# Kernel tuning notes

Measured on AMD Instinct MI355X. Metric: run time of the kernel, lower is better.

Reference implementation:

```python
import jax, jax.numpy as jnp
import numpy as np

B, T, X, E, H, L = 4096, 32, 256, 32, 512, 2  # batch, theta_size, x_size, n_masks, hidden, num_hidden_layers


def _prelu(v, a):
    # PReLU with per-channel slope a (broadcast [E,H] or [B,E,H] vs [B,E,H])
    return jnp.where(v >= 0, v, a * v)


def setup_inputs() -> dict:
    key = jax.random.key(0)
    ks = jax.random.split(key, 12)
    theta = jax.random.normal(ks[0], (B, T), dtype=jnp.float32)
    x = jax.random.normal(ks[1], (B, X), dtype=jnp.float32)
    masks = jax.random.randint(ks[2], (E, T), 0, 2, dtype=jnp.int32)
    masks = masks.at[:, 0].set(1)  # guarantee non-empty subsets
    D = T + X
    s_in = 1.0 / np.sqrt(D)
    s_h = 1.0 / np.sqrt(H)
    # first Linear, split into theta-part and x-part of the weight matrix
    W1t = jax.random.normal(ks[3], (E, T, H), dtype=jnp.float32) * s_in
    W1x = jax.random.normal(ks[4], (E, X, H), dtype=jnp.float32) * s_in
    b1 = jax.random.normal(ks[5], (E, H), dtype=jnp.float32) * s_in
    a1 = jnp.full((E, H), 0.25, dtype=jnp.float32)  # PReLU init
    # num_layers hidden Linear(H,H) + PReLU
    Wh = jax.random.normal(ks[6], (L, E, H, H), dtype=jnp.float32) * s_h
    bh = jax.random.normal(ks[7], (L, E, H), dtype=jnp.float32) * s_h
    ah = jnp.full((L, E, H), 0.25, dtype=jnp.float32)
    # output Linear(H, 1) -> squeeze(-1)
    Wo = jax.random.normal(ks[8], (E, H), dtype=jnp.float32) * s_h
    bo = jax.random.normal(ks[9], (E,), dtype=jnp.float32) * s_h
    return {"theta": theta, "x": x, "masks": masks, "W1t": W1t, "W1x": W1x,
            "b1": b1, "a1": a1, "Wh": Wh, "bh": bh, "ah": ah, "Wo": Wo, "bo": bo}


def reference(theta, x, masks, W1t, W1x, b1, a1, Wh, bh, ah, Wo, bo):
    # theta[..., mask] followed by Linear is equivalent to masking theta per
    # expert and contracting with the full per-expert theta weight block.
    m = masks.astype(theta.dtype)                      # [E, T]
    tm = theta[:, None, :] * m[None, :, :]             # [B, E, T]
    h = (jnp.einsum('bet,eth->beh', tm, W1t)
         + jnp.einsum('bx,exh->beh', x, W1x) + b1)     # [B, E, H]
    h = _prelu(h, a1)
    for i in range(Wh.shape[0]):                       # small fixed layer loop
        h = jnp.einsum('beh,ehk->bek', h, Wh[i]) + bh[i]
        h = _prelu(h, ah[i])
    # Linear(H,1).squeeze(-1), stacked over masks on the last dim -> [B, E]
    return jnp.einsum('beh,eh->be', h, Wo) + bo
```

## Files before the change

### kernel.cpp

```cpp
#include <hip/hip_runtime.h>
#include <stdint.h>

#define B_SZ 4096
#define T_SZ 32
#define X_SZ 256
#define E_SZ 32
#define H_SZ 512
#define BM   64
#define AROW 1040

typedef __attribute__((ext_vector_type(8))) short  short8;
typedef __attribute__((ext_vector_type(4))) float  floatx4;

__device__ __forceinline__ unsigned pk2(float a, float b) {
  unsigned r;
  asm("v_cvt_pk_bf16_f32 %0, %1, %2" : "=v"(r) : "v"(a), "v"(b));
  return r;
}

__global__ __launch_bounds__(256) void prep_kernel(
    const float* __restrict__ W1t, const float* __restrict__ W1x,
    const int* __restrict__ masks, const float* __restrict__ Wh,
    uint4* __restrict__ wcat, uint4* __restrict__ whf) {
  __shared__ unsigned lds[16 * 516];
  const int c = blockIdx.x;
  const int t = threadIdx.x;

  const float* base;
  bool needMask = false;
  int e1 = 0;
  if (c >= 288) {
    int cc = c - 288;
    int le = cc >> 4, kt = cc & 15;
    base = Wh + ((size_t)le * H_SZ + kt * 32) * H_SZ;
  } else {
    int e = c / 9, kt = c - e * 9;
    e1 = e;
    if (kt == 0) { base = W1t + (size_t)e * T_SZ * H_SZ; needMask = true; }
    else          base = W1x + ((size_t)e * X_SZ + (kt - 1) * 32) * H_SZ;
  }

#pragma unroll
  for (int i = 0; i < 8; ++i) {
    int g  = i * 256 + t;
    int k2 = g >> 7, np = g & 127;
    const float* r0 = base + (size_t)(2 * k2) * H_SZ + np * 4;
    float4 a = *(const float4*)r0;
    float4 b = *(const float4*)(r0 + H_SZ);
    if (needMask) {
      float s0 = (float)masks[e1 * T_SZ + 2 * k2];
      float s1 = (float)masks[e1 * T_SZ + 2 * k2 + 1];
      a.x *= s0; a.y *= s0; a.z *= s0; a.w *= s0;
      b.x *= s1; b.y *= s1; b.z *= s1; b.w *= s1;
    }
    *(uint4*)&lds[k2 * 516 + np * 4] =
        make_uint4(pk2(a.x, b.x), pk2(a.y, b.y), pk2(a.z, b.z), pk2(a.w, b.w));
  }
  __syncthreads();

  uint4* outp = (c < 288) ? (wcat + (size_t)c * 2048)
                          : (whf + (size_t)(c - 288) * 2048);
  const int w = t >> 6, l = t & 63, q = l >> 4, l16 = l & 15;
#pragma unroll
  for (int j = 0; j < 8; ++j) {
    int nb = w * 8 + j;
    int n  = nb * 16 + l16;
    int kb = 4 * q;
    uint4 v;
    v.x = lds[(kb + 0) * 516 + n];
    v.y = lds[(kb + 1) * 516 + n];
    v.z = lds[(kb + 2) * 516 + n];
    v.w = lds[(kb + 3) * 516 + n];
    outp[nb * 64 + l] = v;
  }
}

__global__ __launch_bounds__(512, 4) void mlp_kernel(
    const float* __restrict__ theta, const float* __restrict__ x,
    const short8* __restrict__ wcat, const short8* __restrict__ whf,
    const float* __restrict__ b1, const float* __restrict__ a1,
    const float* __restrict__ bh, const float* __restrict__ ah,
    const float* __restrict__ Wo, const float* __restrict__ bo,
    float* __restrict__ out) {
  __shared__ __align__(16) char smA[BM * AROW];
  const int tid = threadIdx.x;
  const int bid = blockIdx.x;
  const int xcd = bid & 7;
  const int t8  = bid >> 3;
  const int e   = xcd * 4 + (t8 >> 6);
  const int m0  = (t8 & 63) * BM;
  const int w   = tid >> 6, l = tid & 63, l16 = l & 15, quad = l >> 4;

  {
    int r = tid >> 3, c = tid & 7;
    float4 th = *(const float4*)(theta + (size_t)(m0 + r) * T_SZ + c * 4);
    *(uint2*)(smA + r * AROW + c * 8) = make_uint2(pk2(th.x, th.y), pk2(th.z, th.w));
    const float4* xp = (const float4*)(x + (size_t)(m0 + r) * X_SZ + c * 32);
#pragma unroll
    for (int q = 0; q < 4; ++q) {
      float4 a = xp[q * 2], b = xp[q * 2 + 1];
      *(uint4*)(smA + r * AROW + 64 + c * 64 + q * 16) =
          make_uint4(pk2(a.x, a.y), pk2(a.z, a.w), pk2(b.x, b.y), pk2(b.z, b.w));
    }
  }
  __syncthreads();

  floatx4 acc[4][4];

  auto gemm = [&](const short8* wbase, int nkt) {
#pragma unroll
    for (int mb = 0; mb < 4; ++mb)
#pragma unroll
      for (int i = 0; i < 4; ++i) acc[mb][i] = (floatx4)(0.f);
    short8 bcur[4], bnxt[4];
    const int boff = w * 256 + l;
#pragma unroll
    for (int i = 0; i < 4; ++i) bcur[i] = wbase[boff + i * 64];
    for (int kt = 0; kt < nkt; ++kt) {
      const short8* wn = wbase + (size_t)(kt + 1 < nkt ? kt + 1 : kt) * 2048;
#pragma unroll
      for (int i = 0; i < 4; ++i) bnxt[i] = wn[boff + i * 64];
      short8 af[4];
#pragma unroll
      for (int mb = 0; mb < 4; ++mb)
        af[mb] = *(const short8*)(smA + (mb * 16 + l16) * AROW + kt * 64 + quad * 16);
#pragma unroll
      for (int mb = 0; mb < 4; ++mb)
#pragma unroll
        for (int i = 0; i < 4; ++i)
          acc[mb][i] = __builtin_amdgcn_mfma_f32_16x16x32_bf16(af[mb], bcur[i],
                                                               acc[mb][i], 0, 0, 0);
#pragma unroll
      for (int i = 0; i < 4; ++i) bcur[i] = bnxt[i];
    }
  };

  auto epi_store = [&](const float* bias, const float* slope) {
    float bb[4], aa[4];
#pragma unroll
    for (int i = 0; i < 4; ++i) {
      int col = w * 64 + i * 16 + l16;
      bb[i] = bias[col];
      aa[i] = slope[col];
    }
    __syncthreads();
#pragma unroll
    for (int mb = 0; mb < 4; ++mb) {
#pragma unroll
      for (int i = 0; i < 4; ++i) {
        unsigned dw[4];
#pragma unroll
        for (int r = 0; r < 4; ++r) {
          float v = acc[mb][i][r] + bb[i];
          v = v >= 0.f ? v : aa[i] * v;
          float o  = __shfl_xor(v, 1, 64);
          float lo = (l16 & 1) ? o : v;
          float hi = (l16 & 1) ? v : o;
          dw[r] = pk2(lo, hi);
        }
        int col2  = w * 64 + i * 16 + (l16 & ~1);
        int rbase = (l16 & 1) * 2;
#pragma unroll
        for (int rr = 0; rr < 2; ++rr) {
          int row = mb * 16 + quad * 4 + rbase + rr;
          *(unsigned*)(smA + row * AROW + col2 * 2) = dw[rbase + rr];
        }
      }
    }
    __syncthreads();
  };

  gemm(wcat + (size_t)e * 9 * 2048, 9);
  epi_store(b1 + (size_t)e * H_SZ, a1 + (size_t)e * H_SZ);
  gemm(whf + (size_t)e * 16 * 2048, 16);
  epi_store(bh + (size_t)e * H_SZ, ah + (size_t)e * H_SZ);
  gemm(whf + (size_t)(E_SZ + e) * 16 * 2048, 16);
  {
    float bb[4], aa[4], wo[4];
#pragma unroll
    for (int i = 0; i < 4; ++i) {
      int col = w * 64 + i * 16 + l16;
      bb[i] = bh[(size_t)(E_SZ + e) * H_SZ + col];
      aa[i] = ah[(size_t)(E_SZ + e) * H_SZ + col];
      wo[i] = Wo[(size_t)e * H_SZ + col];
    }
    float ps[4][4];
#pragma unroll
    for (int mb = 0; mb < 4; ++mb)
#pragma unroll
      for (int r = 0; r < 4; ++r) ps[mb][r] = 0.f;
#pragma unroll
    for (int mb = 0; mb < 4; ++mb)
#pragma unroll
      for (int i = 0; i < 4; ++i)
#pragma unroll
        for (int r = 0; r < 4; ++r) {
          float v = acc[mb][i][r] + bb[i];
          v = v >= 0.f ? v : aa[i] * v;
          ps[mb][r] += v * wo[i];
        }
#pragma unroll
    for (int d = 1; d < 16; d <<= 1)
#pragma unroll
      for (int mb = 0; mb < 4; ++mb)
#pragma unroll
        for (int r = 0; r < 4; ++r) ps[mb][r] += __shfl_xor(ps[mb][r], d, 64);
    __syncthreads();
    float* scratch = (float*)smA;
    if (l16 == 0) {
#pragma unroll
      for (int mb = 0; mb < 4; ++mb)
#pragma unroll
        for (int r = 0; r < 4; ++r)
          scratch[(mb * 16 + quad * 4 + r) * 8 + w] = ps[mb][r];
    }
    __syncthreads();
    if (tid < BM) {
      float s = 0.f;
#pragma unroll
      for (int ww = 0; ww < 8; ++ww) s += scratch[tid * 8 + ww];
      out[(size_t)(m0 + tid) * E_SZ + e] = s + bo[e];
    }
  }
}

extern "C" void kernel_launch(void* const* d_in, const int* in_sizes, int n_in,
                              void* d_out, int out_size, void* d_ws, size_t ws_size,
                              hipStream_t stream) {
  const float* theta = (const float*)d_in[0];
  const float* x     = (const float*)d_in[1];
  const int*   masks = (const int*)d_in[2];
  const float* W1t   = (const float*)d_in[3];
  const float* W1x   = (const float*)d_in[4];
  const float* b1    = (const float*)d_in[5];
  const float* a1    = (const float*)d_in[6];
  const float* Wh    = (const float*)d_in[7];
  const float* bh    = (const float*)d_in[8];
  const float* ah    = (const float*)d_in[9];
  const float* Wo    = (const float*)d_in[10];
  const float* bo    = (const float*)d_in[11];
  float* out = (float*)d_out;

  uint4* wcat = (uint4*)d_ws;
  uint4* whf  = (uint4*)((char*)d_ws + (size_t)E_SZ * 9 * 2048 * 16);

  prep_kernel<<<1312, 256, 0, stream>>>(W1t, W1x, masks, Wh, wcat, whf);
  mlp_kernel<<<2048, 512, 0, stream>>>(theta, x, (const short8*)wcat,
                                       (const short8*)whf, b1, a1, bh, ah, Wo, bo,
                                       out);
}
```

Measured before the change: 319.0 us.

## Stagger per-wave K-loop start and interleave expert block mapping

```diff
diff --git a/kernel.cpp b/kernel.cpp
--- a/kernel.cpp
+++ b/kernel.cpp
@@ -87,8 +87,10 @@
   const int bid = blockIdx.x;
   const int xcd = bid & 7;
   const int t8  = bid >> 3;
-  const int e   = xcd * 4 + (t8 >> 6);
-  const int m0  = (t8 & 63) * BM;
+  const int pr  = t8 >> 7;
+  const int qq  = t8 & 127;
+  const int e   = xcd * 4 + pr * 2 + (qq & 1);
+  const int m0  = (qq >> 1) * BM;
   const int w   = tid >> 6, l = tid & 63, l16 = l & 15, quad = l >> 4;
 
   {
@@ -107,23 +109,28 @@
 
   floatx4 acc[4][4];
 
-  auto gemm = [&](const short8* wbase, int nkt) {
+  auto gemm = [&](const short8* wbase, int nkt, int start) {
 #pragma unroll
     for (int mb = 0; mb < 4; ++mb)
 #pragma unroll
       for (int i = 0; i < 4; ++i) acc[mb][i] = (floatx4)(0.f);
+    const int boff = w * 256 + l;
+    const short8* wp = wbase + (size_t)start * 2048 + boff;
     short8 bcur[4], bnxt[4];
-    const int boff = w * 256 + l;
-#pragma unroll
-    for (int i = 0; i < 4; ++i) bcur[i] = wbase[boff + i * 64];
-    for (int kt = 0; kt < nkt; ++kt) {
-      const short8* wn = wbase + (size_t)(kt + 1 < nkt ? kt + 1 : kt) * 2048;
-#pragma unroll
-      for (int i = 0; i < 4; ++i) bnxt[i] = wn[boff + i * 64];
+#pragma unroll
+    for (int i = 0; i < 4; ++i) bcur[i] = wp[i * 64];
+    int kt = start;
+    const char* arow = smA + l16 * AROW + quad * 16;
+    for (int j = 0; j < nkt; ++j) {
+      int ktn = kt + 1;
+      const short8* wpn = wp + 2048;
+      if (ktn == nkt) { ktn = 0; wpn = wbase + boff; }
+#pragma unroll
+      for (int i = 0; i < 4; ++i) bnxt[i] = wpn[i * 64];
       short8 af[4];
 #pragma unroll
       for (int mb = 0; mb < 4; ++mb)
-        af[mb] = *(const short8*)(smA + (mb * 16 + l16) * AROW + kt * 64 + quad * 16);
+        af[mb] = *(const short8*)(arow + mb * (16 * AROW) + kt * 64);
 #pragma unroll
       for (int mb = 0; mb < 4; ++mb)
 #pragma unroll
@@ -132,6 +139,8 @@
                                                                acc[mb][i], 0, 0, 0);
 #pragma unroll
       for (int i = 0; i < 4; ++i) bcur[i] = bnxt[i];
+      wp = wpn;
+      kt = ktn;
     }
   };
 
@@ -170,11 +179,11 @@
     __syncthreads();
   };
 
-  gemm(wcat + (size_t)e * 9 * 2048, 9);
+  gemm(wcat + (size_t)e * 9 * 2048, 9, (w * 9) >> 3);
   epi_store(b1 + (size_t)e * H_SZ, a1 + (size_t)e * H_SZ);
-  gemm(whf + (size_t)e * 16 * 2048, 16);
+  gemm(whf + (size_t)e * 16 * 2048, 16, w * 2);
   epi_store(bh + (size_t)e * H_SZ, ah + (size_t)e * H_SZ);
-  gemm(whf + (size_t)(E_SZ + e) * 16 * 2048, 16);
+  gemm(whf + (size_t)(E_SZ + e) * 16 * 2048, 16, w * 2);
   {
     float bb[4], aa[4], wo[4];
 #pragma unroll
```

After: 321.5 us. About the same (+0.8%).

## Double row tile to 128 and fully unroll GEMM with ping-pong weight buffers

Applied to the files above, without the earlier changes.

```diff
diff --git a/kernel.cpp b/kernel.cpp
--- a/kernel.cpp
+++ b/kernel.cpp
@@ -1,12 +1,13 @@
 #include <hip/hip_runtime.h>
 #include <stdint.h>
+#include <type_traits>
 
 #define B_SZ 4096
 #define T_SZ 32
 #define X_SZ 256
 #define E_SZ 32
 #define H_SZ 512
-#define BM   64
+#define BM   128
 #define AROW 1040
 
 typedef __attribute__((ext_vector_type(8))) short  short8;
@@ -75,7 +76,7 @@
   }
 }
 
-__global__ __launch_bounds__(512, 4) void mlp_kernel(
+__global__ __launch_bounds__(512, 2) void mlp_kernel(
     const float* __restrict__ theta, const float* __restrict__ x,
     const short8* __restrict__ wcat, const short8* __restrict__ whf,
     const float* __restrict__ b1, const float* __restrict__ a1,
@@ -87,51 +88,69 @@
   const int bid = blockIdx.x;
   const int xcd = bid & 7;
   const int t8  = bid >> 3;
-  const int e   = xcd * 4 + (t8 >> 6);
-  const int m0  = (t8 & 63) * BM;
+  const int e   = xcd * 4 + (t8 >> 5);
+  const int m0  = (t8 & 31) * BM;
   const int w   = tid >> 6, l = tid & 63, l16 = l & 15, quad = l >> 4;
 
   {
-    int r = tid >> 3, c = tid & 7;
-    float4 th = *(const float4*)(theta + (size_t)(m0 + r) * T_SZ + c * 4);
-    *(uint2*)(smA + r * AROW + c * 8) = make_uint2(pk2(th.x, th.y), pk2(th.z, th.w));
-    const float4* xp = (const float4*)(x + (size_t)(m0 + r) * X_SZ + c * 32);
-#pragma unroll
-    for (int q = 0; q < 4; ++q) {
-      float4 a = xp[q * 2], b = xp[q * 2 + 1];
-      *(uint4*)(smA + r * AROW + 64 + c * 64 + q * 16) =
+    int r = tid >> 2, c = tid & 3;
+    const float* tp = theta + (size_t)(m0 + r) * T_SZ + c * 8;
+    float4 t0 = *(const float4*)tp;
+    float4 t1 = *(const float4*)(tp + 4);
+    *(uint4*)(smA + r * AROW + c * 16) =
+        make_uint4(pk2(t0.x, t0.y), pk2(t0.z, t0.w), pk2(t1.x, t1.y), pk2(t1.z, t1.w));
+    const float* xp = x + (size_t)(m0 + r) * X_SZ + c * 64;
+#pragma unroll
+    for (int j = 0; j < 8; ++j) {
+      float4 a = *(const float4*)(xp + j * 8);
+      float4 b = *(const float4*)(xp + j * 8 + 4);
+      *(uint4*)(smA + r * AROW + 64 + c * 128 + j * 16) =
           make_uint4(pk2(a.x, a.y), pk2(a.z, a.w), pk2(b.x, b.y), pk2(b.z, b.w));
     }
   }
   __syncthreads();
 
-  floatx4 acc[4][4];
-
-  auto gemm = [&](const short8* wbase, int nkt) {
-#pragma unroll
-    for (int mb = 0; mb < 4; ++mb)
+  floatx4 acc[8][4];
+  const int u0 = w * 256 + l;
+  const char* ar0 = smA + l16 * AROW + quad * 16;
+  const char* ar1 = ar0 + 4 * 16 * AROW;
+
+  auto gemm = [&](const short8* wbase, auto nktc) {
+    constexpr int NKT = decltype(nktc)::value;
+#pragma unroll
+    for (int mb = 0; mb < 8; ++mb)
 #pragma unroll
       for (int i = 0; i < 4; ++i) acc[mb][i] = (floatx4)(0.f);
-    short8 bcur[4], bnxt[4];
-    const int boff = w * 256 + l;
-#pragma unroll
-    for (int i = 0; i < 4; ++i) bcur[i] = wbase[boff + i * 64];
-    for (int kt = 0; kt < nkt; ++kt) {
-      const short8* wn = wbase + (size_t)(kt + 1 < nkt ? kt + 1 : kt) * 2048;
-#pragma unroll
-      for (int i = 0; i < 4; ++i) bnxt[i] = wn[boff + i * 64];
-      short8 af[4];
+    const short8* wu = wbase;
+    short8 bA[4], bB[4];
+#pragma unroll
+    for (int i = 0; i < 4; ++i) bA[i] = wu[u0 + i * 64];
+#pragma unroll
+    for (int kt = 0; kt < NKT; ++kt) {
+      if (kt + 1 < NKT) {
+        const short8* wn = wu + 2048;
+        if (kt & 1) {
+#pragma unroll
+          for (int i = 0; i < 4; ++i) bA[i] = wn[u0 + i * 64];
+        } else {
+#pragma unroll
+          for (int i = 0; i < 4; ++i) bB[i] = wn[u0 + i * 64];
+        }
+      }
+      short8 af[8];
 #pragma unroll
       for (int mb = 0; mb < 4; ++mb)
-        af[mb] = *(const short8*)(smA + (mb * 16 + l16) * AROW + kt * 64 + quad * 16);
+        af[mb] = *(const short8*)(ar0 + mb * (16 * AROW) + kt * 64);
 #pragma unroll
       for (int mb = 0; mb < 4; ++mb)
+        af[mb + 4] = *(const short8*)(ar1 + mb * (16 * AROW) + kt * 64);
+#pragma unroll
+      for (int mb = 0; mb < 8; ++mb)
 #pragma unroll
         for (int i = 0; i < 4; ++i)
-          acc[mb][i] = __builtin_amdgcn_mfma_f32_16x16x32_bf16(af[mb], bcur[i],
-                                                               acc[mb][i], 0, 0, 0);
-#pragma unroll
-      for (int i = 0; i < 4; ++i) bcur[i] = bnxt[i];
+          acc[mb][i] = __builtin_amdgcn_mfma_f32_16x16x32_bf16(
+              af[mb], (kt & 1) ? bB[i] : bA[i], acc[mb][i], 0, 0, 0);
+      wu += 2048;
     }
   };
 
@@ -145,7 +164,7 @@
     }
     __syncthreads();
 #pragma unroll
-    for (int mb = 0; mb < 4; ++mb) {
+    for (int mb = 0; mb < 8; ++mb) {
 #pragma unroll
       for (int i = 0; i < 4; ++i) {
         unsigned dw[4];
@@ -170,11 +189,11 @@
     __syncthreads();
   };
 
-  gemm(wcat + (size_t)e * 9 * 2048, 9);
+  gemm(wcat + (size_t)e * 9 * 2048, std::integral_constant<int, 9>{});
   epi_store(b1 + (size_t)e * H_SZ, a1 + (size_t)e * H_SZ);
-  gemm(whf + (size_t)e * 16 * 2048, 16);
+  gemm(whf + (size_t)e * 16 * 2048, std::integral_constant<int, 16>{});
   epi_store(bh + (size_t)e * H_SZ, ah + (size_t)e * H_SZ);
-  gemm(whf + (size_t)(E_SZ + e) * 16 * 2048, 16);
+  gemm(whf + (size_t)(E_SZ + e) * 16 * 2048, std::integral_constant<int, 16>{});
   {
     float bb[4], aa[4], wo[4];
 #pragma unroll
@@ -184,13 +203,13 @@
       aa[i] = ah[(size_t)(E_SZ + e) * H_SZ + col];
       wo[i] = Wo[(size_t)e * H_SZ + col];
     }
-    float ps[4][4];
-#pragma unroll
-    for (int mb = 0; mb < 4; ++mb)
+    float ps[8][4];
+#pragma unroll
+    for (int mb = 0; mb < 8; ++mb)
 #pragma unroll
       for (int r = 0; r < 4; ++r) ps[mb][r] = 0.f;
 #pragma unroll
-    for (int mb = 0; mb < 4; ++mb)
+    for (int mb = 0; mb < 8; ++mb)
 #pragma unroll
       for (int i = 0; i < 4; ++i)
 #pragma unroll
@@ -202,14 +221,14 @@
 #pragma unroll
     for (int d = 1; d < 16; d <<= 1)
 #pragma unroll
-      for (int mb = 0; mb < 4; ++mb)
+      for (int mb = 0; mb < 8; ++mb)
 #pragma unroll
         for (int r = 0; r < 4; ++r) ps[mb][r] += __shfl_xor(ps[mb][r], d, 64);
     __syncthreads();
     float* scratch = (float*)smA;
     if (l16 == 0) {
 #pragma unroll
-      for (int mb = 0; mb < 4; ++mb)
+      for (int mb = 0; mb < 8; ++mb)
 #pragma unroll
         for (int r = 0; r < 4; ++r)
           scratch[(mb * 16 + quad * 4 + r) * 8 + w] = ps[mb][r];
@@ -245,7 +264,7 @@
   uint4* whf  = (uint4*)((char*)d_ws + (size_t)E_SZ * 9 * 2048 * 16);
 
   prep_kernel<<<1312, 256, 0, stream>>>(W1t, W1x, masks, Wh, wcat, whf);
-  mlp_kernel<<<2048, 512, 0, stream>>>(theta, x, (const short8*)wcat,
+  mlp_kernel<<<1024, 512, 0, stream>>>(theta, x, (const short8*)wcat,
                                        (const short8*)whf, b1, a1, bh, ah, Wo, bo,
                                        out);
 }
```

New measurement: 343.5 us. 7.7% more time.
